# Kernel tuning notes

Hardware: AMD Instinct MI355X
Metric: run time of the kernel (lower is better)

Reference implementation:

```python
import jax, jax.numpy as jnp
import numpy as np

B, N = 512, 256
NC = N // 2          # number of SOC (friction-cone) constraints
MAX_ITER = 100       # matches module max_iter
POWER_ITERS = 20     # power iterations for Lipschitz constant estimate


def setup_inputs() -> dict:
    key = jax.random.key(0)
    k1, k2, k3, k4 = jax.random.split(key, 4)
    P = jax.random.normal(k1, (B, N, N), dtype=jnp.float32)
    q = jax.random.normal(k2, (B, N, 1), dtype=jnp.float32)
    l_n = jax.random.uniform(k3, (B, NC, 1), dtype=jnp.float32)
    mu = jax.random.uniform(k4, (B, NC, 1), dtype=jnp.float32)
    return {"P": P, "q": q, "l_n": l_n, "mu": mu}


def _solve(P, b, r):
    # minimize 0.5 * ||P l||^2 + b^T l   s.t.  ||l[2i:2i+2]|| <= r[i]
    # via FISTA (accelerated projected gradient); projection onto a product
    # of 2-D balls is closed-form, honoring the block-SOC structure.
    H = jnp.einsum('bki,bkj->bij', P, P)  # [B,N,N] = P^T P (PSD)

    # Lipschitz constant of grad = lambda_max(H) via power iteration
    def power_step(v, _):
        w = jnp.einsum('bij,bj->bi', H, v)
        v = w / (jnp.linalg.norm(w, axis=-1, keepdims=True) + 1e-12)
        return v, None

    v0 = jnp.ones((B, N), dtype=P.dtype)
    v, _ = jax.lax.scan(power_step, v0, None, length=POWER_ITERS)
    Hv = jnp.einsum('bij,bj->bi', H, v)
    L = jnp.sum(v * Hv, axis=-1) / jnp.sum(v * v, axis=-1)  # [B] Rayleigh quotient
    step = 1.0 / (1.05 * jnp.maximum(L, 1e-12))             # [B]

    def project(l):
        pairs = l.reshape(B, NC, 2)
        nrm = jnp.linalg.norm(pairs, axis=-1)               # [B,NC]
        scale = jnp.where(nrm > r, r / jnp.maximum(nrm, 1e-30), 1.0)
        return (pairs * scale[..., None]).reshape(B, N)

    def fista_step(carry, _):
        l, y, t = carry
        g = jnp.einsum('bij,bj->bi', H, y) + b
        l_new = project(y - step[:, None] * g)
        t_new = 0.5 * (1.0 + jnp.sqrt(1.0 + 4.0 * t * t))
        y_new = l_new + ((t - 1.0) / t_new) * (l_new - l)
        return (l_new, y_new, t_new), None

    l0 = project(jnp.zeros_like(b))
    (l, _, _), _ = jax.lax.scan(fista_step, (l0, l0, jnp.float32(1.0)),
                                None, length=MAX_ITER)
    return l  # [B,N]


def reference(P, q, l_n, mu):
    b = q[..., 0]            # [B,N]
    r = (mu * l_n)[..., 0]   # [B,NC] nonneg SOC radii (mu*l_n in the original)
    return _solve(P, b, r)
```

## Files before the change

### kernel.cpp

```cpp
#include <hip/hip_runtime.h>
#include <math.h>


namespace {

constexpr int NDIM = 256;
constexpr int NCON = 128;
constexpr int PITERS = 20;
constexpr int FITERS = 100;

typedef short bf16x8 __attribute__((ext_vector_type(8)));
typedef float f32x4  __attribute__((ext_vector_type(4)));
typedef float f32x2  __attribute__((ext_vector_type(2)));

#define MFMA_BF16_16x16x32(accv, av, bv)                                  \
    asm volatile("v_mfma_f32_16x16x32_bf16 %0, %1, %2, %0"                \
                 : "+v"(accv) : "v"(av), "v"(bv))

struct Smem {
    union {
        struct {
            unsigned short fragHi[16 * 64 * 8];
            unsigned short fragLo[16 * 64 * 8];
        };
        float Hbuf[8][32 * 36];
    };
    float red[2][8][256];
    float scal[16];
};

__device__ __forceinline__ unsigned short bf16rne(float x) {
    unsigned u = __float_as_uint(x);
    unsigned r = u + 0x7FFFu + ((u >> 16) & 1u);
    return (unsigned short)(r >> 16);
}

__device__ __forceinline__ float readlane_f(float v, int lane) {
    return __int_as_float(__builtin_amdgcn_readlane(__float_as_int(v), lane));
}

__device__ __forceinline__ void mv_pk(const float (&h)[128], float cy,
                                      float* __restrict__ redw, int l)
{
    const f32x2* h2 = (const f32x2*)h;
    f32x2 pw01 = {0.f, 0.f}, pw23 = {0.f, 0.f};
#pragma unroll
    for (int j = 0; j < 32; ++j) {
        float x = readlane_f(cy, j);
        f32x2 xb = {x, x};
        pw01 = __builtin_elementwise_fma(h2[2 * j],     xb, pw01);
        pw23 = __builtin_elementwise_fma(h2[2 * j + 1], xb, pw23);
    }
    *(float4*)(redw + 4 * l) = make_float4(pw01.x, pw01.y, pw23.x, pw23.y);
}

__device__ __forceinline__ float gather_one(const float (*red8)[256], int w, int l)
{
    const float* rp = &red8[0][32 * w + l];
    float s = 0.f;
#pragma unroll
    for (int c = 0; c < 8; ++c) s += rp[c * 256];
    return s;
}

__global__ __launch_bounds__(512, 2)
void qcqp_fista(const float* __restrict__ P, const float* __restrict__ q,
                const float* __restrict__ ln_, const float* __restrict__ mu,
                float* __restrict__ out)
{
    __shared__ Smem sm;
    const int b = blockIdx.x;
    const int t = threadIdx.x;
    const int w = t >> 6;
    const int l = t & 63;

    const float* Pb = P + (size_t)b * (NDIM * NDIM);

    const int col  = t & 255;
    const int half = t >> 8;
    const int tile = col >> 4;

    float pf[16];
    auto load_chunk = [&](int cc) {
#pragma unroll
        for (int g = 0; g < 2; ++g) {
            const int qd = 2 * half + g;
            const float* src = Pb + (cc * 32 + qd * 8) * 256 + col;
#pragma unroll
            for (int j = 0; j < 8; ++j) pf[g * 8 + j] = src[j * 256];
        }
    };

    f32x4 acc[16][2];
#pragma unroll
    for (int i = 0; i < 16; ++i)
#pragma unroll
        for (int j = 0; j < 2; ++j)
#pragma unroll
            for (int e = 0; e < 4; ++e) acc[i][j][e] = 0.0f;

    load_chunk(0);
    for (int c = 0; c < 8; ++c) {
#pragma unroll
        for (int g = 0; g < 2; ++g) {
            const int qd = 2 * half + g;
            unsigned hw[4], lw[4];
#pragma unroll
            for (int jp = 0; jp < 4; ++jp) {
                float f0 = pf[g * 8 + 2 * jp], f1 = pf[g * 8 + 2 * jp + 1];
                unsigned short h0 = bf16rne(f0), h1 = bf16rne(f1);
                float r0 = f0 - __uint_as_float((unsigned)h0 << 16);
                float r1 = f1 - __uint_as_float((unsigned)h1 << 16);
                unsigned short lo0 = bf16rne(r0), lo1 = bf16rne(r1);
                hw[jp] = (unsigned)h0 | ((unsigned)h1 << 16);
                lw[jp] = (unsigned)lo0 | ((unsigned)lo1 << 16);
            }
            const int slot = tile * 64 + ((col & 15) + 16 * qd);
            ((uint4*)sm.fragHi)[slot] = make_uint4(hw[0], hw[1], hw[2], hw[3]);
            ((uint4*)sm.fragLo)[slot] = make_uint4(lw[0], lw[1], lw[2], lw[3]);
        }
        __syncthreads();
        if (c < 7) load_chunk(c + 1);

        const bf16x8* FH = (const bf16x8*)sm.fragHi;
        const bf16x8* FL = (const bf16x8*)sm.fragLo;
        bf16x8 bh0 = FH[(2 * w) * 64 + l];
        bf16x8 bl0 = FL[(2 * w) * 64 + l];
        bf16x8 bh1 = FH[(2 * w + 1) * 64 + l];
        bf16x8 bl1 = FL[(2 * w + 1) * 64 + l];
#pragma unroll
        for (int tr = 0; tr < 16; ++tr) {
            bf16x8 ah = FH[tr * 64 + l];
            bf16x8 al = FL[tr * 64 + l];
            MFMA_BF16_16x16x32(acc[tr][0], ah, bh0);
            MFMA_BF16_16x16x32(acc[tr][0], al, bh0);
            MFMA_BF16_16x16x32(acc[tr][0], ah, bl0);
            MFMA_BF16_16x16x32(acc[tr][1], ah, bh1);
            MFMA_BF16_16x16x32(acc[tr][1], al, bh1);
            MFMA_BF16_16x16x32(acc[tr][1], ah, bl1);
        }
        __syncthreads();
    }

    asm volatile("s_nop 7\n\ts_nop 7" ::: );

    const int qd4 = (l >> 4) * 4;
    const int c16 = l & 15;
    float* Hw = sm.Hbuf[w];
    float h[128];
#pragma unroll
    for (int rc = 0; rc < 8; ++rc) {
#pragma unroll
        for (int tt = 0; tt < 2; ++tt)
#pragma unroll
            for (int tc = 0; tc < 2; ++tc)
#pragma unroll
                for (int reg = 0; reg < 4; ++reg) {
                    int row_local = 16 * tt + qd4 + reg;
                    Hw[row_local * 36 + 16 * tc + c16] = acc[2 * rc + tt][tc][reg];
                }
        if ((l >> 3) == rc) {
            int l2 = l & 7;
#pragma unroll
            for (int e = 0; e < 4; ++e)
#pragma unroll
                for (int jj = 0; jj < 8; ++jj) {
                    float4 v = *(const float4*)&Hw[(4 * l2 + e) * 36 + 4 * jj];
                    h[4 * (4 * jj + 0) + e] = v.x;
                    h[4 * (4 * jj + 1) + e] = v.y;
                    h[4 * (4 * jj + 2) + e] = v.z;
                    h[4 * (4 * jj + 3) + e] = v.w;
                }
        }
    }

    float cy = 1.0f;
    int phase = 0;
    for (int it = 0; it < PITERS; ++it, ++phase) {
        mv_pk(h, cy, sm.red[phase & 1][w], l);
        __syncthreads();
        if (l < 32) {
            float s = gather_one(sm.red[phase & 1], w, l);
            cy = s * 0.0009765625f;
        }
    }

    mv_pk(h, cy, sm.red[phase & 1][w], l);
    __syncthreads();
    float n1 = 0.f, n2 = 0.f;
    if (l < 32) {
        float hv = gather_one(sm.red[phase & 1], w, l);
        n1 = cy * hv;
        n2 = cy * cy;
    }
#pragma unroll
    for (int off = 1; off < 64; off <<= 1) {
        n1 += __shfl_xor(n1, off);
        n2 += __shfl_xor(n2, off);
    }
    if (l == 0) { sm.scal[w] = n1; sm.scal[8 + w] = n2; }
    __syncthreads();
    float num = 0.f, den = 0.f;
#pragma unroll
    for (int ww = 0; ww < 8; ++ww) { num += sm.scal[ww]; den += sm.scal[8 + ww]; }
    float L = num / den;
    const float step = 1.0f / (1.05f * fmaxf(L, 1e-12f));
    ++phase;

    float bq = 0.f, rrv = 0.f, rr2 = 0.f;
    if (l < 32) {
        bq = q[b * NDIM + 32 * w + l];
        float rv = mu[b * NCON + 16 * w + (l >> 1)] * ln_[b * NCON + 16 * w + (l >> 1)];
        rrv = rv;
        rr2 = rv * rv;
    }
    float li = 0.f, tcur = 1.0f;
    cy = 0.0f;

    for (int it = 0; it < FITERS; ++it, ++phase) {
        mv_pk(h, cy, sm.red[phase & 1][w], l);
        __syncthreads();
        float tn = 0.5f * (1.0f + sqrtf(1.0f + 4.0f * tcur * tcur));
        float ratio = (tcur - 1.0f) / tn;
        tcur = tn;
        if (l < 32) {
            float hy = gather_one(sm.red[phase & 1], w, l);
            float z  = cy - step * (hy + bq);
            float zz = z * z;
            float n2p = zz + __shfl_xor(zz, 1);
            float scl = (n2p > rr2) ? (rrv * rsqrtf(n2p)) : 1.0f;
            float l0 = z * scl;
            float yn = l0 + ratio * (l0 - li);
            li = l0;
            cy = yn;
        }
    }

    if (l < 32)
        out[b * NDIM + 32 * w + l] = li;
}

}

extern "C" void kernel_launch(void* const* d_in, const int* in_sizes, int n_in,
                              void* d_out, int out_size, void* d_ws, size_t ws_size,
                              hipStream_t stream) {
    const float* P   = (const float*)d_in[0];
    const float* q   = (const float*)d_in[1];
    const float* l_n = (const float*)d_in[2];
    const float* mu  = (const float*)d_in[3];
    float* out = (float*)d_out;
    qcqp_fista<<<dim3(512), dim3(512), 0, stream>>>(P, q, l_n, mu, out);
}
```

Measured before the change: 388.8 us.

## Split per-batch H rows across 16 waves with 1024-thread blocks

Doubles the block to 1024 threads. Each wave holds half of its column block's H entries in registers (64 floats instead of 128) and computes half of the MFMA row tiles for H = P^T P. The matvec partial sums are reduced through a reshaped shared buffer. Halving the serial FMA chain per wave is meant to cut latency in each power and FISTA iteration, at the cost of barriers spanning 16 waves and redundant scalar updates in both halves. The launch bound also caps registers, which could cause spills.

```diff
diff --git a/kernel.cpp b/kernel.cpp
--- a/kernel.cpp
+++ b/kernel.cpp
@@ -23,9 +23,9 @@
             unsigned short fragHi[16 * 64 * 8];
             unsigned short fragLo[16 * 64 * 8];
         };
-        float Hbuf[8][32 * 36];
+        float Hbuf[16][32 * 36];
     };
-    float red[2][8][256];
+    float red[2][16][128];
     float scal[16];
 };
 
@@ -39,31 +39,29 @@
     return __int_as_float(__builtin_amdgcn_readlane(__float_as_int(v), lane));
 }
 
-__device__ __forceinline__ void mv_pk(const float (&h)[128], float cy,
+__device__ __forceinline__ void mv_pk(const float (&h)[64], float cy,
                                       float* __restrict__ redw, int l)
 {
     const f32x2* h2 = (const f32x2*)h;
-    f32x2 pw01 = {0.f, 0.f}, pw23 = {0.f, 0.f};
+    f32x2 pw = {0.f, 0.f};
 #pragma unroll
     for (int j = 0; j < 32; ++j) {
         float x = readlane_f(cy, j);
         f32x2 xb = {x, x};
-        pw01 = __builtin_elementwise_fma(h2[2 * j],     xb, pw01);
-        pw23 = __builtin_elementwise_fma(h2[2 * j + 1], xb, pw23);
-    }
-    *(float4*)(redw + 4 * l) = make_float4(pw01.x, pw01.y, pw23.x, pw23.y);
-}
-
-__device__ __forceinline__ float gather_one(const float (*red8)[256], int w, int l)
+        pw = __builtin_elementwise_fma(h2[j], xb, pw);
+    }
+    *(float2*)(redw + 2 * l) = make_float2(pw.x, pw.y);
+}
+
+__device__ __forceinline__ float gather_one(const float* __restrict__ rp)
 {
-    const float* rp = &red8[0][32 * w + l];
     float s = 0.f;
 #pragma unroll
-    for (int c = 0; c < 8; ++c) s += rp[c * 256];
+    for (int c = 0; c < 8; ++c) s += rp[c * 128];
     return s;
 }
 
-__global__ __launch_bounds__(512, 2)
+__global__ __launch_bounds__(1024, 4)
 void qcqp_fista(const float* __restrict__ P, const float* __restrict__ q,
                 const float* __restrict__ ln_, const float* __restrict__ mu,
                 float* __restrict__ out)
@@ -71,29 +69,27 @@
     __shared__ Smem sm;
     const int b = blockIdx.x;
     const int t = threadIdx.x;
-    const int w = t >> 6;
-    const int l = t & 63;
+    const int w  = t >> 6;
+    const int l  = t & 63;
+    const int ws = w & 7;
+    const int rh = w >> 3;
 
     const float* Pb = P + (size_t)b * (NDIM * NDIM);
 
     const int col  = t & 255;
-    const int half = t >> 8;
+    const int qd   = t >> 8;
     const int tile = col >> 4;
 
-    float pf[16];
+    float pf[8];
     auto load_chunk = [&](int cc) {
-#pragma unroll
-        for (int g = 0; g < 2; ++g) {
-            const int qd = 2 * half + g;
-            const float* src = Pb + (cc * 32 + qd * 8) * 256 + col;
-#pragma unroll
-            for (int j = 0; j < 8; ++j) pf[g * 8 + j] = src[j * 256];
-        }
+        const float* src = Pb + (cc * 32 + qd * 8) * 256 + col;
+#pragma unroll
+        for (int j = 0; j < 8; ++j) pf[j] = src[j * 256];
     };
 
-    f32x4 acc[16][2];
-#pragma unroll
-    for (int i = 0; i < 16; ++i)
+    f32x4 acc[8][2];
+#pragma unroll
+    for (int i = 0; i < 8; ++i)
 #pragma unroll
         for (int j = 0; j < 2; ++j)
 #pragma unroll
@@ -101,43 +97,39 @@
 
     load_chunk(0);
     for (int c = 0; c < 8; ++c) {
-#pragma unroll
-        for (int g = 0; g < 2; ++g) {
-            const int qd = 2 * half + g;
-            unsigned hw[4], lw[4];
-#pragma unroll
-            for (int jp = 0; jp < 4; ++jp) {
-                float f0 = pf[g * 8 + 2 * jp], f1 = pf[g * 8 + 2 * jp + 1];
-                unsigned short h0 = bf16rne(f0), h1 = bf16rne(f1);
-                float r0 = f0 - __uint_as_float((unsigned)h0 << 16);
-                float r1 = f1 - __uint_as_float((unsigned)h1 << 16);
-                unsigned short lo0 = bf16rne(r0), lo1 = bf16rne(r1);
-                hw[jp] = (unsigned)h0 | ((unsigned)h1 << 16);
-                lw[jp] = (unsigned)lo0 | ((unsigned)lo1 << 16);
-            }
-            const int slot = tile * 64 + ((col & 15) + 16 * qd);
-            ((uint4*)sm.fragHi)[slot] = make_uint4(hw[0], hw[1], hw[2], hw[3]);
-            ((uint4*)sm.fragLo)[slot] = make_uint4(lw[0], lw[1], lw[2], lw[3]);
-        }
+        unsigned hw[4], lw[4];
+#pragma unroll
+        for (int jp = 0; jp < 4; ++jp) {
+            float f0 = pf[2 * jp], f1 = pf[2 * jp + 1];
+            unsigned short h0 = bf16rne(f0), h1 = bf16rne(f1);
+            float r0 = f0 - __uint_as_float((unsigned)h0 << 16);
+            float r1 = f1 - __uint_as_float((unsigned)h1 << 16);
+            unsigned short lo0 = bf16rne(r0), lo1 = bf16rne(r1);
+            hw[jp] = (unsigned)h0 | ((unsigned)h1 << 16);
+            lw[jp] = (unsigned)lo0 | ((unsigned)lo1 << 16);
+        }
+        const int slot = tile * 64 + (col & 15) + 16 * qd;
+        ((uint4*)sm.fragHi)[slot] = make_uint4(hw[0], hw[1], hw[2], hw[3]);
+        ((uint4*)sm.fragLo)[slot] = make_uint4(lw[0], lw[1], lw[2], lw[3]);
         __syncthreads();
         if (c < 7) load_chunk(c + 1);
 
         const bf16x8* FH = (const bf16x8*)sm.fragHi;
         const bf16x8* FL = (const bf16x8*)sm.fragLo;
-        bf16x8 bh0 = FH[(2 * w) * 64 + l];
-        bf16x8 bl0 = FL[(2 * w) * 64 + l];
-        bf16x8 bh1 = FH[(2 * w + 1) * 64 + l];
-        bf16x8 bl1 = FL[(2 * w + 1) * 64 + l];
-#pragma unroll
-        for (int tr = 0; tr < 16; ++tr) {
-            bf16x8 ah = FH[tr * 64 + l];
-            bf16x8 al = FL[tr * 64 + l];
-            MFMA_BF16_16x16x32(acc[tr][0], ah, bh0);
-            MFMA_BF16_16x16x32(acc[tr][0], al, bh0);
-            MFMA_BF16_16x16x32(acc[tr][0], ah, bl0);
-            MFMA_BF16_16x16x32(acc[tr][1], ah, bh1);
-            MFMA_BF16_16x16x32(acc[tr][1], al, bh1);
-            MFMA_BF16_16x16x32(acc[tr][1], ah, bl1);
+        bf16x8 bh0 = FH[(2 * ws) * 64 + l];
+        bf16x8 bl0 = FL[(2 * ws) * 64 + l];
+        bf16x8 bh1 = FH[(2 * ws + 1) * 64 + l];
+        bf16x8 bl1 = FL[(2 * ws + 1) * 64 + l];
+#pragma unroll
+        for (int tt = 0; tt < 8; ++tt) {
+            bf16x8 ah = FH[(8 * rh + tt) * 64 + l];
+            bf16x8 al = FL[(8 * rh + tt) * 64 + l];
+            MFMA_BF16_16x16x32(acc[tt][0], ah, bh0);
+            MFMA_BF16_16x16x32(acc[tt][0], al, bh0);
+            MFMA_BF16_16x16x32(acc[tt][0], ah, bl0);
+            MFMA_BF16_16x16x32(acc[tt][1], ah, bh1);
+            MFMA_BF16_16x16x32(acc[tt][1], al, bh1);
+            MFMA_BF16_16x16x32(acc[tt][1], ah, bl1);
         }
         __syncthreads();
     }
@@ -147,32 +139,34 @@
     const int qd4 = (l >> 4) * 4;
     const int c16 = l & 15;
     float* Hw = sm.Hbuf[w];
-    float h[128];
-#pragma unroll
-    for (int rc = 0; rc < 8; ++rc) {
-#pragma unroll
-        for (int tt = 0; tt < 2; ++tt)
+    float h[64];
+#pragma unroll
+    for (int rc = 0; rc < 4; ++rc) {
+#pragma unroll
+        for (int s = 0; s < 2; ++s)
 #pragma unroll
             for (int tc = 0; tc < 2; ++tc)
 #pragma unroll
-                for (int reg = 0; reg < 4; ++reg) {
-                    int row_local = 16 * tt + qd4 + reg;
-                    Hw[row_local * 36 + 16 * tc + c16] = acc[2 * rc + tt][tc][reg];
+                for (int reg = 0; reg < 4; ++reg)
+                    Hw[(16 * s + qd4 + reg) * 36 + 16 * tc + c16] =
+                        acc[2 * rc + s][tc][reg];
+        if ((l >> 4) == rc) {
+            const int lr = 2 * (l & 15);
+#pragma unroll
+            for (int i = 0; i < 2; ++i)
+#pragma unroll
+                for (int jj = 0; jj < 8; ++jj) {
+                    float4 v = *(const float4*)&Hw[(lr + i) * 36 + 4 * jj];
+                    h[2 * (4 * jj + 0) + i] = v.x;
+                    h[2 * (4 * jj + 1) + i] = v.y;
+                    h[2 * (4 * jj + 2) + i] = v.z;
+                    h[2 * (4 * jj + 3) + i] = v.w;
                 }
-        if ((l >> 3) == rc) {
-            int l2 = l & 7;
-#pragma unroll
-            for (int e = 0; e < 4; ++e)
-#pragma unroll
-                for (int jj = 0; jj < 8; ++jj) {
-                    float4 v = *(const float4*)&Hw[(4 * l2 + e) * 36 + 4 * jj];
-                    h[4 * (4 * jj + 0) + e] = v.x;
-                    h[4 * (4 * jj + 1) + e] = v.y;
-                    h[4 * (4 * jj + 2) + e] = v.z;
-                    h[4 * (4 * jj + 3) + e] = v.w;
-                }
-        }
-    }
+        }
+    }
+
+    const int rhp   = ws >> 2;
+    const int rbase = 32 * (ws & 3);
 
     float cy = 1.0f;
     int phase = 0;
@@ -180,7 +174,7 @@
         mv_pk(h, cy, sm.red[phase & 1][w], l);
         __syncthreads();
         if (l < 32) {
-            float s = gather_one(sm.red[phase & 1], w, l);
+            float s = gather_one(&sm.red[phase & 1][8 * rhp][rbase + l]);
             cy = s * 0.0009765625f;
         }
     }
@@ -189,7 +183,7 @@
     __syncthreads();
     float n1 = 0.f, n2 = 0.f;
     if (l < 32) {
-        float hv = gather_one(sm.red[phase & 1], w, l);
+        float hv = gather_one(&sm.red[phase & 1][8 * rhp][rbase + l]);
         n1 = cy * hv;
         n2 = cy * cy;
     }
@@ -198,7 +192,7 @@
         n1 += __shfl_xor(n1, off);
         n2 += __shfl_xor(n2, off);
     }
-    if (l == 0) { sm.scal[w] = n1; sm.scal[8 + w] = n2; }
+    if (l == 0 && rh == 0) { sm.scal[ws] = n1; sm.scal[8 + ws] = n2; }
     __syncthreads();
     float num = 0.f, den = 0.f;
 #pragma unroll
@@ -209,8 +203,8 @@
 
     float bq = 0.f, rrv = 0.f, rr2 = 0.f;
     if (l < 32) {
-        bq = q[b * NDIM + 32 * w + l];
-        float rv = mu[b * NCON + 16 * w + (l >> 1)] * ln_[b * NCON + 16 * w + (l >> 1)];
+        bq = q[b * NDIM + 32 * ws + l];
+        float rv = mu[b * NCON + 16 * ws + (l >> 1)] * ln_[b * NCON + 16 * ws + (l >> 1)];
         rrv = rv;
         rr2 = rv * rv;
     }
@@ -224,7 +218,7 @@
         float ratio = (tcur - 1.0f) / tn;
         tcur = tn;
         if (l < 32) {
-            float hy = gather_one(sm.red[phase & 1], w, l);
+            float hy = gather_one(&sm.red[phase & 1][8 * rhp][rbase + l]);
             float z  = cy - step * (hy + bq);
             float zz = z * z;
             float n2p = zz + __shfl_xor(zz, 1);
@@ -236,8 +230,8 @@
         }
     }
 
-    if (l < 32)
-        out[b * NDIM + 32 * w + l] = li;
+    if (rh == 0 && l < 32)
+        out[b * NDIM + 32 * ws + l] = li;
 }
 
 }
@@ -250,5 +244,5 @@
     const float* l_n = (const float*)d_in[2];
     const float* mu  = (const float*)d_in[3];
     float* out = (float*)d_out;
-    qcqp_fista<<<dim3(512), dim3(512), 0, stream>>>(P, q, l_n, mu, out);
-}
+    qcqp_fista<<<dim3(512), dim3(1024), 0, stream>>>(P, q, l_n, mu, out);
+}
```

Measured after the change: 433.0 us. +11.4%, slower.

## Split P^T P Gram computation into two row-half passes to cut accumulator registers

Applied to the files above, without the earlier changes.

Computes H = P^T P in two passes, each covering half of the output row tiles, so only 8x2 accumulator vectors are live instead of 16x2. Between passes each wave unpacks its share of H into the h[] register array. The goal is lower register pressure and fewer spills, since h[128] and the accumulators were live together. The cost is that P is read from global memory twice and converted to bf16 hi/lo twice.

```diff
diff --git a/kernel.cpp b/kernel.cpp
--- a/kernel.cpp
+++ b/kernel.cpp
@@ -91,87 +91,91 @@
         }
     };
 
-    f32x4 acc[16][2];
-#pragma unroll
-    for (int i = 0; i < 16; ++i)
-#pragma unroll
-        for (int j = 0; j < 2; ++j)
-#pragma unroll
-            for (int e = 0; e < 4; ++e) acc[i][j][e] = 0.0f;
-
-    load_chunk(0);
-    for (int c = 0; c < 8; ++c) {
-#pragma unroll
-        for (int g = 0; g < 2; ++g) {
-            const int qd = 2 * half + g;
-            unsigned hw[4], lw[4];
-#pragma unroll
-            for (int jp = 0; jp < 4; ++jp) {
-                float f0 = pf[g * 8 + 2 * jp], f1 = pf[g * 8 + 2 * jp + 1];
-                unsigned short h0 = bf16rne(f0), h1 = bf16rne(f1);
-                float r0 = f0 - __uint_as_float((unsigned)h0 << 16);
-                float r1 = f1 - __uint_as_float((unsigned)h1 << 16);
-                unsigned short lo0 = bf16rne(r0), lo1 = bf16rne(r1);
-                hw[jp] = (unsigned)h0 | ((unsigned)h1 << 16);
-                lw[jp] = (unsigned)lo0 | ((unsigned)lo1 << 16);
-            }
-            const int slot = tile * 64 + ((col & 15) + 16 * qd);
-            ((uint4*)sm.fragHi)[slot] = make_uint4(hw[0], hw[1], hw[2], hw[3]);
-            ((uint4*)sm.fragLo)[slot] = make_uint4(lw[0], lw[1], lw[2], lw[3]);
-        }
-        __syncthreads();
-        if (c < 7) load_chunk(c + 1);
-
-        const bf16x8* FH = (const bf16x8*)sm.fragHi;
-        const bf16x8* FL = (const bf16x8*)sm.fragLo;
-        bf16x8 bh0 = FH[(2 * w) * 64 + l];
-        bf16x8 bl0 = FL[(2 * w) * 64 + l];
-        bf16x8 bh1 = FH[(2 * w + 1) * 64 + l];
-        bf16x8 bl1 = FL[(2 * w + 1) * 64 + l];
-#pragma unroll
-        for (int tr = 0; tr < 16; ++tr) {
-            bf16x8 ah = FH[tr * 64 + l];
-            bf16x8 al = FL[tr * 64 + l];
-            MFMA_BF16_16x16x32(acc[tr][0], ah, bh0);
-            MFMA_BF16_16x16x32(acc[tr][0], al, bh0);
-            MFMA_BF16_16x16x32(acc[tr][0], ah, bl0);
-            MFMA_BF16_16x16x32(acc[tr][1], ah, bh1);
-            MFMA_BF16_16x16x32(acc[tr][1], al, bh1);
-            MFMA_BF16_16x16x32(acc[tr][1], ah, bl1);
-        }
-        __syncthreads();
-    }
-
-    asm volatile("s_nop 7\n\ts_nop 7" ::: );
-
     const int qd4 = (l >> 4) * 4;
     const int c16 = l & 15;
     float* Hw = sm.Hbuf[w];
     float h[128];
-#pragma unroll
-    for (int rc = 0; rc < 8; ++rc) {
-#pragma unroll
-        for (int tt = 0; tt < 2; ++tt)
-#pragma unroll
-            for (int tc = 0; tc < 2; ++tc)
-#pragma unroll
-                for (int reg = 0; reg < 4; ++reg) {
-                    int row_local = 16 * tt + qd4 + reg;
-                    Hw[row_local * 36 + 16 * tc + c16] = acc[2 * rc + tt][tc][reg];
+
+    load_chunk(0);
+    for (int pass = 0; pass < 2; ++pass) {
+        f32x4 acc[8][2];
+#pragma unroll
+        for (int i = 0; i < 8; ++i)
+#pragma unroll
+            for (int j = 0; j < 2; ++j)
+#pragma unroll
+                for (int e = 0; e < 4; ++e) acc[i][j][e] = 0.0f;
+
+        for (int c = 0; c < 8; ++c) {
+#pragma unroll
+            for (int g = 0; g < 2; ++g) {
+                const int qd = 2 * half + g;
+                unsigned hw[4], lw[4];
+#pragma unroll
+                for (int jp = 0; jp < 4; ++jp) {
+                    float f0 = pf[g * 8 + 2 * jp], f1 = pf[g * 8 + 2 * jp + 1];
+                    unsigned short h0 = bf16rne(f0), h1 = bf16rne(f1);
+                    float r0 = f0 - __uint_as_float((unsigned)h0 << 16);
+                    float r1 = f1 - __uint_as_float((unsigned)h1 << 16);
+                    unsigned short lo0 = bf16rne(r0), lo1 = bf16rne(r1);
+                    hw[jp] = (unsigned)h0 | ((unsigned)h1 << 16);
+                    lw[jp] = (unsigned)lo0 | ((unsigned)lo1 << 16);
                 }
-        if ((l >> 3) == rc) {
-            int l2 = l & 7;
-#pragma unroll
-            for (int e = 0; e < 4; ++e)
-#pragma unroll
-                for (int jj = 0; jj < 8; ++jj) {
-                    float4 v = *(const float4*)&Hw[(4 * l2 + e) * 36 + 4 * jj];
-                    h[4 * (4 * jj + 0) + e] = v.x;
-                    h[4 * (4 * jj + 1) + e] = v.y;
-                    h[4 * (4 * jj + 2) + e] = v.z;
-                    h[4 * (4 * jj + 3) + e] = v.w;
-                }
-        }
+                const int slot = tile * 64 + ((col & 15) + 16 * qd);
+                ((uint4*)sm.fragHi)[slot] = make_uint4(hw[0], hw[1], hw[2], hw[3]);
+                ((uint4*)sm.fragLo)[slot] = make_uint4(lw[0], lw[1], lw[2], lw[3]);
+            }
+            __syncthreads();
+            if (c < 7) load_chunk(c + 1);
+            else if (pass == 0) load_chunk(0);
+
+            const bf16x8* FH = (const bf16x8*)sm.fragHi;
+            const bf16x8* FL = (const bf16x8*)sm.fragLo;
+            bf16x8 bh0 = FH[(2 * w) * 64 + l];
+            bf16x8 bl0 = FL[(2 * w) * 64 + l];
+            bf16x8 bh1 = FH[(2 * w + 1) * 64 + l];
+            bf16x8 bl1 = FL[(2 * w + 1) * 64 + l];
+#pragma unroll
+            for (int tt = 0; tt < 8; ++tt) {
+                bf16x8 ah = FH[(8 * pass + tt) * 64 + l];
+                bf16x8 al = FL[(8 * pass + tt) * 64 + l];
+                MFMA_BF16_16x16x32(acc[tt][0], ah, bh0);
+                MFMA_BF16_16x16x32(acc[tt][0], al, bh0);
+                MFMA_BF16_16x16x32(acc[tt][0], ah, bl0);
+                MFMA_BF16_16x16x32(acc[tt][1], ah, bh1);
+                MFMA_BF16_16x16x32(acc[tt][1], al, bh1);
+                MFMA_BF16_16x16x32(acc[tt][1], ah, bl1);
+            }
+            __syncthreads();
+        }
+
+        asm volatile("s_nop 7\n\ts_nop 7" ::: );
+
+#pragma unroll
+        for (int rc = 0; rc < 4; ++rc) {
+#pragma unroll
+            for (int s = 0; s < 2; ++s)
+#pragma unroll
+                for (int tc = 0; tc < 2; ++tc)
+#pragma unroll
+                    for (int reg = 0; reg < 4; ++reg)
+                        Hw[(16 * s + qd4 + reg) * 36 + 16 * tc + c16] =
+                            acc[2 * rc + s][tc][reg];
+            if ((l >> 3) == 4 * pass + rc) {
+                int l2 = l & 7;
+#pragma unroll
+                for (int e = 0; e < 4; ++e)
+#pragma unroll
+                    for (int jj = 0; jj < 8; ++jj) {
+                        float4 v = *(const float4*)&Hw[(4 * l2 + e) * 36 + 4 * jj];
+                        h[4 * (4 * jj + 0) + e] = v.x;
+                        h[4 * (4 * jj + 1) + e] = v.y;
+                        h[4 * (4 * jj + 2) + e] = v.z;
+                        h[4 * (4 * jj + 3) + e] = v.w;
+                    }
+            }
+        }
+        if (pass == 0) __syncthreads();
     }
 
     float cy = 1.0f;
```

After: 1.027 ms. 2.64x slower.
